# Optimization experiments

Measured on AMD Instinct MI355X. Metric: run time of the kernel, lower is better.

## Reference

```python
import jax, jax.numpy as jnp
import numpy as np

B, S, D = 2, 2048, 1024
N_HEAD, D_ATTN = 16, 64


def setup_inputs() -> dict:
    key = jax.random.key(0)
    ks = jax.random.split(key, 5)
    x = jax.random.normal(ks[0], (B, S, D), dtype=jnp.float32)
    # causal mask: True = masked (as consumed by torch.masked_fill)
    mask = jnp.triu(jnp.ones((S, S), dtype=bool), k=1)
    scale = 0.02
    w_q = jax.random.normal(ks[1], (D, N_HEAD * D_ATTN), dtype=jnp.float32) * scale
    w_k = jax.random.normal(ks[2], (D, N_HEAD * D_ATTN), dtype=jnp.float32) * scale
    w_v = jax.random.normal(ks[3], (D, N_HEAD * D_ATTN), dtype=jnp.float32) * scale
    w_o = jax.random.normal(ks[4], (N_HEAD * D_ATTN, D), dtype=jnp.float32) * scale
    return {"x": x, "mask": mask, "w_q": w_q, "w_k": w_k, "w_v": w_v, "w_o": w_o}


def _split(t):
    # [B,S,H*Da] -> [B,H,S,Da]
    b, s, _ = t.shape
    return t.reshape(b, s, N_HEAD, D_ATTN).transpose(0, 2, 1, 3)


def reference(x, mask, w_q, w_k, w_v, w_o):
    q = _split(x @ w_q)
    k = _split(x @ w_k)
    v = _split(x @ w_v)
    scale = D_ATTN ** 0.5
    score = jnp.einsum("bhqd,bhkd->bhqk", q, k) / scale  # [B,H,S,S]
    score = jnp.where(mask, -jnp.inf, score)
    prob = jax.nn.softmax(score, axis=-1)
    out = jnp.einsum("bhqk,bhkd->bhqd", prob, v)
    out = out.transpose(0, 2, 1, 3).reshape(x.shape[0], x.shape[1], N_HEAD * D_ATTN)
    return out @ w_o
```

## Files before the change

### kernel.cpp

```cpp
#include <hip/hip_runtime.h>
#include <stdint.h>

using u16 = unsigned short;
using u32 = unsigned int;
using u64 = unsigned long long;

typedef float f32x4 __attribute__((ext_vector_type(4)));
typedef __bf16 bf16x8 __attribute__((ext_vector_type(8)));

#define DEV static __device__ __forceinline__

DEV u16 f2bf(float f) {
  u32 u = __float_as_uint(f);
  u += 0x7FFFu + ((u >> 16) & 1u);
  return (u16)(u >> 16);
}

DEV void gld16(const void* g, void* l) {
  __builtin_amdgcn_global_load_lds((__attribute__((address_space(1))) void*)g,
                                   (__attribute__((address_space(3))) void*)l,
                                   16, 0, 0);
}

__global__ void k_cvt_x(const float* __restrict__ x, u16* __restrict__ xb) {
  int i = (blockIdx.x * 256 + threadIdx.x) * 8;
  float4 a = *(const float4*)&x[i];
  float4 b = *(const float4*)&x[i + 4];
  __align__(16) u16 o[8];
  o[0] = f2bf(a.x); o[1] = f2bf(a.y); o[2] = f2bf(a.z); o[3] = f2bf(a.w);
  o[4] = f2bf(b.x); o[5] = f2bf(b.y); o[6] = f2bf(b.z); o[7] = f2bf(b.w);
  *(uint4*)&xb[i] = *(const uint4*)o;
}

__global__ void k_cvt_w(const float* __restrict__ w0, const float* __restrict__ w1,
                        const float* __restrict__ w2, const float* __restrict__ w3,
                        u16* __restrict__ t0, u16* __restrict__ t1,
                        u16* __restrict__ t2, u16* __restrict__ t3) {
  const float* w = blockIdx.z == 0 ? w0 : blockIdx.z == 1 ? w1 : blockIdx.z == 2 ? w2 : w3;
  u16* wt       = blockIdx.z == 0 ? t0 : blockIdx.z == 1 ? t1 : blockIdx.z == 2 ? t2 : t3;
  __shared__ __align__(16) float tile[64][68];
  const int tid = threadIdx.x;
  const int k0 = blockIdx.x * 64, n0 = blockIdx.y * 64;
#pragma unroll
  for (int i = 0; i < 4; ++i) {
    int c = tid + i * 256;
    int kr = c >> 4, col = (c & 15) * 4;
    *(float4*)&tile[kr][col] = *(const float4*)&w[(size_t)(k0 + kr) * 1024 + n0 + col];
  }
  __syncthreads();
#pragma unroll
  for (int i = 0; i < 2; ++i) {
    int c = tid + i * 256;
    int nr = c >> 3, kc = (c & 7) * 8;
    __align__(16) u16 o[8];
#pragma unroll
    for (int j = 0; j < 8; ++j) o[j] = f2bf(tile[kc + j][nr]);
    *(uint4*)&wt[(size_t)(n0 + nr) * 1024 + k0 + kc] = *(const uint4*)o;
  }
}

DEV void gemm_mainloop(const u16* __restrict__ A, const u16* __restrict__ Bt,
                       int m0, int n0, u16* Asb, u16* Bsb, f32x4 (&acc)[4][4]) {
  const int tid = threadIdx.x;
  const int lane = tid & 63;
  const int wv = tid >> 6;
  const int wm = (wv >> 1) * 64, wn = (wv & 1) * 64;

#pragma unroll
  for (int i = 0; i < 4; ++i)
#pragma unroll
    for (int j = 0; j < 4; ++j) {
      f32x4 z = {0.f, 0.f, 0.f, 0.f};
      acc[i][j] = z;
    }

  const int c0 = wv * 64 + lane, c1 = c0 + 256;
  const int r0 = c0 >> 2, r1 = c1 >> 2;
  const int b0 = (c0 & 3) ^ (r0 & 3) ^ ((r0 >> 2) & 3);
  const int b1 = (c1 & 3) ^ (r1 & 3) ^ ((r1 >> 2) & 3);
  const u16* ga0 = A + (size_t)(m0 + r0) * 1024 + b0 * 8;
  const u16* ga1 = A + (size_t)(m0 + r1) * 1024 + b1 * 8;
  const u16* gb0 = Bt + (size_t)(n0 + r0) * 1024 + b0 * 8;
  const u16* gb1 = Bt + (size_t)(n0 + r1) * 1024 + b1 * 8;
  u16* la0 = Asb + (wv * 64) * 8;
  u16* la1 = Asb + (wv * 64 + 256) * 8;
  u16* lb0 = Bsb + (wv * 64) * 8;
  u16* lb1 = Bsb + (wv * 64 + 256) * 8;

  int aoff[4], boff[4];
#pragma unroll
  for (int f = 0; f < 4; ++f) {
    int ra = wm + f * 16 + (lane & 15);
    aoff[f] = ra * 32 + (((lane >> 4) ^ (ra & 3) ^ ((ra >> 2) & 3)) * 8);
    int rb = wn + f * 16 + (lane & 15);
    boff[f] = rb * 32 + (((lane >> 4) ^ (rb & 3) ^ ((rb >> 2) & 3)) * 8);
  }

  for (int kt = 0; kt < 32; ++kt) {
    const int k0 = kt * 32;
    gld16(ga0 + k0, la0);
    gld16(ga1 + k0, la1);
    gld16(gb0 + k0, lb0);
    gld16(gb1 + k0, lb1);
    __syncthreads();
    bf16x8 af[4], bfv[4];
#pragma unroll
    for (int f = 0; f < 4; ++f) af[f] = *(const bf16x8*)&Asb[aoff[f]];
#pragma unroll
    for (int f = 0; f < 4; ++f) bfv[f] = *(const bf16x8*)&Bsb[boff[f]];
#pragma unroll
    for (int i = 0; i < 4; ++i)
#pragma unroll
      for (int j = 0; j < 4; ++j)
        acc[i][j] = __builtin_amdgcn_mfma_f32_16x16x32_bf16(af[i], bfv[j], acc[i][j], 0, 0, 0);
    __syncthreads();
  }
}

__global__ __launch_bounds__(256) void k_gemm_qkv(
    const u16* __restrict__ X, const u16* __restrict__ Wq, const u16* __restrict__ Wk,
    const u16* __restrict__ Wv, u16* __restrict__ Q, u16* __restrict__ K,
    u16* __restrict__ V) {
  __shared__ __align__(16) u16 Asb[128 * 32];
  __shared__ __align__(16) u16 Bsb[128 * 32];
  const int nb = blockIdx.x, mb = blockIdx.y;
  const int proj = nb >> 3, n0 = (nb & 7) * 128;
  const u16* W = proj == 0 ? Wq : proj == 1 ? Wk : Wv;
  u16* Dst = proj == 0 ? Q : proj == 1 ? K : V;
  const float scl = proj == 0 ? 0.125f * 1.4426950408889634f : 1.0f;
  f32x4 acc[4][4];
  gemm_mainloop(X, W, mb * 128, n0, Asb, Bsb, acc);
  const int lane = threadIdx.x & 63, wv = threadIdx.x >> 6;
  const int wm = (wv >> 1) * 64, wn = (wv & 1) * 64;
#pragma unroll
  for (int i = 0; i < 4; ++i)
#pragma unroll
    for (int j = 0; j < 4; ++j)
#pragma unroll
      for (int r = 0; r < 4; ++r) {
        int m = mb * 128 + wm + i * 16 + (lane >> 4) * 4 + r;
        int n = n0 + wn + j * 16 + (lane & 15);
        int b = m >> 11, s = m & 2047, h = n >> 6, d = n & 63;
        Dst[(size_t)((b * 16 + h) * 2048 + s) * 64 + d] = f2bf(acc[i][j][r] * scl);
      }
}

__global__ __launch_bounds__(256) void k_gemm_out(
    const u16* __restrict__ A, const u16* __restrict__ Wt, float* __restrict__ Out) {
  __shared__ __align__(16) u16 Asb[128 * 32];
  __shared__ __align__(16) u16 Bsb[128 * 32];
  const int nb = blockIdx.x, mb = blockIdx.y;
  f32x4 acc[4][4];
  gemm_mainloop(A, Wt, mb * 128, nb * 128, Asb, Bsb, acc);
  const int lane = threadIdx.x & 63, wv = threadIdx.x >> 6;
  const int wm = (wv >> 1) * 64, wn = (wv & 1) * 64;
#pragma unroll
  for (int i = 0; i < 4; ++i)
#pragma unroll
    for (int j = 0; j < 4; ++j)
#pragma unroll
      for (int r = 0; r < 4; ++r) {
        int m = mb * 128 + wm + i * 16 + (lane >> 4) * 4 + r;
        int n = nb * 128 + wn + j * 16 + (lane & 15);
        Out[(size_t)m * 1024 + n] = acc[i][j][r];
      }
}

__global__ void k_transpose_v(const u16* __restrict__ V, u16* __restrict__ Vt) {
  __shared__ __align__(16) u16 t[64][80];
  const int bh = blockIdx.y, s0 = blockIdx.x * 64;
  const int tid = threadIdx.x;
#pragma unroll
  for (int i = 0; i < 2; ++i) {
    int c = tid + i * 256;
    int sr = c >> 3, dc = (c & 7) * 8;
    *(uint4*)&t[sr][dc] = *(const uint4*)&V[((size_t)bh * 2048 + s0 + sr) * 64 + dc];
  }
  __syncthreads();
#pragma unroll
  for (int i = 0; i < 2; ++i) {
    int c = tid + i * 256;
    int dr = c >> 3, c7 = c & 7;
    __align__(8) u16 o[8];
#pragma unroll
    for (int j = 0; j < 8; ++j) o[j] = t[c7 * 8 + j][dr];
    int bp = ((c7 >> 1) & 1) * 32 + (c7 & 1) * 16 + ((c7 >> 2) & 1) * 4;
    u16* row = &Vt[((size_t)bh * 64 + dr) * 2048 + s0];
    *(u64*)&row[bp]     = *(const u64*)&o[0];
    *(u64*)&row[bp + 8] = *(const u64*)&o[4];
  }
}

DEV void qk_tile(const u16* Kc, const bf16x8 (&qf)[2], int lo, int hi, f32x4 (&sc)[4]) {
#pragma unroll
  for (int cf = 0; cf < 4; ++cf) {
    f32x4 z = {0.f, 0.f, 0.f, 0.f};
    sc[cf] = z;
#pragma unroll
    for (int kf = 0; kf < 2; ++kf) {
      int row = cf * 16 + lo;
      int blk = ((kf * 4 + hi) ^ (row & 7)) * 8;
      bf16x8 kfr = *(const bf16x8*)&Kc[row * 64 + blk];
      sc[cf] = __builtin_amdgcn_mfma_f32_16x16x32_bf16(kfr, qf[kf], sc[cf], 0, 0, 0);
    }
  }
}

DEV void sm_pv(f32x4 (&sc)[4], const u16* Vc, int lane, int lo, int hi,
               float& m_run, float& l_run, f32x4 (&ao)[4]) {
  float mx0 = fmaxf(fmaxf(sc[0][0], sc[0][1]), fmaxf(sc[0][2], sc[0][3]));
  float mx1 = fmaxf(fmaxf(sc[1][0], sc[1][1]), fmaxf(sc[1][2], sc[1][3]));
  float mx2 = fmaxf(fmaxf(sc[2][0], sc[2][1]), fmaxf(sc[2][2], sc[2][3]));
  float mx3 = fmaxf(fmaxf(sc[3][0], sc[3][1]), fmaxf(sc[3][2], sc[3][3]));
  float mx = fmaxf(fmaxf(mx0, mx1), fmaxf(mx2, mx3));
  mx = fmaxf(mx, __shfl_xor(mx, 16));
  mx = fmaxf(mx, __shfl_xor(mx, 32));

  if (__any(mx > m_run + 8.0f)) {
    float mnew = fmaxf(m_run, mx);
    float sclf = __builtin_amdgcn_exp2f(m_run - mnew);
    const int base = lane & 48;
#pragma unroll
    for (int r = 0; r < 4; ++r) {
      float s_r = __shfl(sclf, base + hi * 4 + r);
#pragma unroll
      for (int df = 0; df < 4; ++df) ao[df][r] *= s_r;
    }
    l_run *= sclf;
    m_run = mnew;
  }

  float pp[4];
  bf16x8 pa0, pa1;
#pragma unroll
  for (int cf = 0; cf < 4; ++cf) {
    float p0 = __builtin_amdgcn_exp2f(sc[cf][0] - m_run);
    float p1 = __builtin_amdgcn_exp2f(sc[cf][1] - m_run);
    float p2 = __builtin_amdgcn_exp2f(sc[cf][2] - m_run);
    float p3 = __builtin_amdgcn_exp2f(sc[cf][3] - m_run);
    pp[cf] = (p0 + p1) + (p2 + p3);
    bf16x8& pa = (cf & 1) ? pa1 : pa0;
    int j = (cf >> 1) * 4;
    pa[j] = (__bf16)p0; pa[j + 1] = (__bf16)p1;
    pa[j + 2] = (__bf16)p2; pa[j + 3] = (__bf16)p3;
  }
  float psum = (pp[0] + pp[1]) + (pp[2] + pp[3]);
  psum += __shfl_xor(psum, 16);
  psum += __shfl_xor(psum, 32);
  l_run += psum;

  __builtin_amdgcn_s_setprio(1);
#pragma unroll
  for (int df = 0; df < 4; ++df) {
#pragma unroll
    for (int kf = 0; kf < 2; ++kf) {
      int row = df * 16 + lo;
      int blk = ((kf * 4 + hi) ^ (row & 7)) * 8;
      bf16x8 vfr = *(const bf16x8*)&Vc[row * 64 + blk];
      ao[df] = __builtin_amdgcn_mfma_f32_16x16x32_bf16(kf == 0 ? pa0 : pa1, vfr,
                                                       ao[df], 0, 0, 0);
    }
  }
  __builtin_amdgcn_s_setprio(0);
}

__global__ __launch_bounds__(512) void k_attn(
    const u16* __restrict__ Qg, const u16* __restrict__ Kg,
    const u16* __restrict__ Vtg, u16* __restrict__ Og) {
  __shared__ __align__(16) u16 Ks[2][64 * 64];
  __shared__ __align__(16) u16 Vs[2][64 * 64];
  const int tid = threadIdx.x, lane = tid & 63, wv = tid >> 6;
  const int lo = lane & 15, hi = lane >> 4;
  const int w4 = wv & 3, qsel = wv >> 2;

  const int flat = blockIdx.y * 16 + blockIdx.x;
  const int xcd = flat & 7, slot = flat >> 3;
  const int bh = xcd * 4 + (slot >> 4);
  const int jp = slot & 15;

  const u16* Qb = Qg + (size_t)bh * 2048 * 64;
  const u16* Kb = Kg + (size_t)bh * 2048 * 64;
  const u16* Vb = Vtg + (size_t)bh * 64 * 2048;
  const int b = bh >> 4, h = bh & 15;

  const int nta = jp + 1, ntb = 32 - jp;
  const int q0 = (qsel ? (31 - jp) : jp) * 64;
  const int myNt = qsel ? ntb : nta;
  const int qq = q0 + w4 * 16 + lo;

  bf16x8 qf[2];
#pragma unroll
  for (int kf = 0; kf < 2; ++kf)
    qf[kf] = *(const bf16x8*)&Qb[(size_t)(q0 + w4 * 16 + lo) * 64 + kf * 32 + hi * 8];

  f32x4 ao[4];
#pragma unroll
  for (int df = 0; df < 4; ++df) {
    f32x4 z = {0.f, 0.f, 0.f, 0.f};
    ao[df] = z;
  }
  float m_run = -1e30f, l_run = 0.f;

  const int r0 = tid >> 3;
  const int e0 = ((tid & 7) ^ (r0 & 7)) * 8;

  gld16(Kb + (size_t)r0 * 64 + e0, &Ks[0][wv * 512]);
  gld16(Vb + (size_t)r0 * 2048 + e0, &Vs[0][wv * 512]);
  __syncthreads();

#pragma unroll 1
  for (int t = 0; t < ntb; ++t) {
    const u16* Kc = Ks[t & 1];
    const u16* Vc = Vs[t & 1];
    if (t + 1 < ntb) {
      const int kn = (t + 1) * 64;
      gld16(Kb + (size_t)(kn + r0) * 64 + e0, &Ks[(t + 1) & 1][wv * 512]);
      gld16(Vb + (size_t)r0 * 2048 + kn + e0, &Vs[(t + 1) & 1][wv * 512]);
    }

    if (t < myNt) {
      f32x4 sc[4];
      __builtin_amdgcn_s_setprio(1);
      qk_tile(Kc, qf, lo, hi, sc);
      __builtin_amdgcn_s_setprio(0);

      if (t == myNt - 1) {
        const int kv0 = t * 64;
#pragma unroll
        for (int cf = 0; cf < 4; ++cf)
#pragma unroll
          for (int r = 0; r < 4; ++r) {
            int kk = kv0 + cf * 16 + hi * 4 + r;
            if (kk > qq) sc[cf][r] = -1e30f;
          }
      }

      sm_pv(sc, Vc, lane, lo, hi, m_run, l_run, ao);
    }

    __syncthreads();
  }

  float linv[4];
  const int base = lane & 48;
#pragma unroll
  for (int r = 0; r < 4; ++r) {
    float l_r = __shfl(l_run, base + hi * 4 + r);
    linv[r] = 1.0f / l_r;
  }
#pragma unroll
  for (int df = 0; df < 4; ++df)
#pragma unroll
    for (int r = 0; r < 4; ++r) {
      int s = q0 + w4 * 16 + hi * 4 + r;
      int d = df * 16 + lo;
      Og[((size_t)(b * 2048 + s)) * 1024 + h * 64 + d] = f2bf(ao[df][r] * linv[r]);
    }
}

extern "C" void kernel_launch(void* const* d_in, const int* in_sizes, int n_in,
                              void* d_out, int out_size, void* d_ws, size_t ws_size,
                              hipStream_t stream) {
  const float* x = (const float*)d_in[0];
  const float* wq = (const float*)d_in[2];
  const float* wk = (const float*)d_in[3];
  const float* wv = (const float*)d_in[4];
  const float* wo = (const float*)d_in[5];

  char* ws = (char*)d_ws;
  u16* xb  = (u16*)(ws);
  u16* wqt = (u16*)(ws + 8388608);
  u16* wkt = (u16*)(ws + 8388608 + 2097152);
  u16* wvt = (u16*)(ws + 8388608 + 2 * 2097152);
  u16* wot = (u16*)(ws + 8388608 + 3 * 2097152);
  u16* qb  = (u16*)(ws + 16777216);
  u16* kb  = (u16*)(ws + 16777216 + 8388608);
  u16* vb  = (u16*)(ws + 16777216 + 2 * 8388608);
  u16* vt  = (u16*)(ws + 16777216 + 3 * 8388608);
  u16* ao  = (u16*)(ws + 16777216 + 4 * 8388608);

  k_cvt_x<<<dim3(2048), dim3(256), 0, stream>>>(x, xb);
  k_cvt_w<<<dim3(16, 16, 4), dim3(256), 0, stream>>>(wq, wk, wv, wo, wqt, wkt, wvt, wot);
  k_gemm_qkv<<<dim3(24, 32), dim3(256), 0, stream>>>(xb, wqt, wkt, wvt, qb, kb, vb);
  k_transpose_v<<<dim3(32, 32), dim3(256), 0, stream>>>(vb, vt);
  k_attn<<<dim3(16, 32), dim3(512), 0, stream>>>(qb, kb, vt, ao);
  k_gemm_out<<<dim3(8, 32), dim3(256), 0, stream>>>(ao, wot, (float*)d_out);
}
```

Measured before the change: 122.9 us.

## Give each attention wave two query row-fragments and merge conversion kernels

The attention kernel drops from 512 to 256 threads per block. Each wave now processes 32 query rows as two 16-row fragments, so every K and V fragment read from LDS feeds two MFMAs and LDS traffic per FLOP is halved. Each thread issues twice as many async tile loads, and registers per thread roughly double for accumulators, scores and Q fragments, which may limit occupancy. Separately, the x and weight bf16 conversion kernels are merged into one launch to save a kernel launch.

```diff
diff --git a/kernel.cpp b/kernel.cpp
--- a/kernel.cpp
+++ b/kernel.cpp
@@ -22,36 +22,39 @@
                                    16, 0, 0);
 }
 
-__global__ void k_cvt_x(const float* __restrict__ x, u16* __restrict__ xb) {
-  int i = (blockIdx.x * 256 + threadIdx.x) * 8;
-  float4 a = *(const float4*)&x[i];
-  float4 b = *(const float4*)&x[i + 4];
-  __align__(16) u16 o[8];
-  o[0] = f2bf(a.x); o[1] = f2bf(a.y); o[2] = f2bf(a.z); o[3] = f2bf(a.w);
-  o[4] = f2bf(b.x); o[5] = f2bf(b.y); o[6] = f2bf(b.z); o[7] = f2bf(b.w);
-  *(uint4*)&xb[i] = *(const uint4*)o;
-}
-
-__global__ void k_cvt_w(const float* __restrict__ w0, const float* __restrict__ w1,
-                        const float* __restrict__ w2, const float* __restrict__ w3,
-                        u16* __restrict__ t0, u16* __restrict__ t1,
-                        u16* __restrict__ t2, u16* __restrict__ t3) {
-  const float* w = blockIdx.z == 0 ? w0 : blockIdx.z == 1 ? w1 : blockIdx.z == 2 ? w2 : w3;
-  u16* wt       = blockIdx.z == 0 ? t0 : blockIdx.z == 1 ? t1 : blockIdx.z == 2 ? t2 : t3;
+__global__ void k_cvt(const float* __restrict__ x, u16* __restrict__ xb,
+                      const float* __restrict__ w0, const float* __restrict__ w1,
+                      const float* __restrict__ w2, const float* __restrict__ w3,
+                      u16* __restrict__ t0, u16* __restrict__ t1,
+                      u16* __restrict__ t2, u16* __restrict__ t3) {
+  const int tid = threadIdx.x;
+  if (blockIdx.x < 2048) {
+    int i = (blockIdx.x * 256 + tid) * 8;
+    float4 a = *(const float4*)&x[i];
+    float4 b = *(const float4*)&x[i + 4];
+    __align__(16) u16 o[8];
+    o[0] = f2bf(a.x); o[1] = f2bf(a.y); o[2] = f2bf(a.z); o[3] = f2bf(a.w);
+    o[4] = f2bf(b.x); o[5] = f2bf(b.y); o[6] = f2bf(b.z); o[7] = f2bf(b.w);
+    *(uint4*)&xb[i] = *(const uint4*)o;
+    return;
+  }
+  const int c = blockIdx.x - 2048;
+  const int z = c >> 8, rem = c & 255;
+  const float* w = z == 0 ? w0 : z == 1 ? w1 : z == 2 ? w2 : w3;
+  u16* wt       = z == 0 ? t0 : z == 1 ? t1 : z == 2 ? t2 : t3;
   __shared__ __align__(16) float tile[64][68];
-  const int tid = threadIdx.x;
-  const int k0 = blockIdx.x * 64, n0 = blockIdx.y * 64;
+  const int k0 = (rem & 15) * 64, n0 = (rem >> 4) * 64;
 #pragma unroll
   for (int i = 0; i < 4; ++i) {
-    int c = tid + i * 256;
-    int kr = c >> 4, col = (c & 15) * 4;
+    int cc = tid + i * 256;
+    int kr = cc >> 4, col = (cc & 15) * 4;
     *(float4*)&tile[kr][col] = *(const float4*)&w[(size_t)(k0 + kr) * 1024 + n0 + col];
   }
   __syncthreads();
 #pragma unroll
   for (int i = 0; i < 2; ++i) {
-    int c = tid + i * 256;
-    int nr = c >> 3, kc = (c & 7) * 8;
+    int cc = tid + i * 256;
+    int nr = cc >> 3, kc = (cc & 7) * 8;
     __align__(16) u16 o[8];
 #pragma unroll
     for (int j = 0; j < 8; ++j) o[j] = f2bf(tile[kc + j][nr]);
@@ -191,87 +194,14 @@
   }
 }
 
-DEV void qk_tile(const u16* Kc, const bf16x8 (&qf)[2], int lo, int hi, f32x4 (&sc)[4]) {
-#pragma unroll
-  for (int cf = 0; cf < 4; ++cf) {
-    f32x4 z = {0.f, 0.f, 0.f, 0.f};
-    sc[cf] = z;
-#pragma unroll
-    for (int kf = 0; kf < 2; ++kf) {
-      int row = cf * 16 + lo;
-      int blk = ((kf * 4 + hi) ^ (row & 7)) * 8;
-      bf16x8 kfr = *(const bf16x8*)&Kc[row * 64 + blk];
-      sc[cf] = __builtin_amdgcn_mfma_f32_16x16x32_bf16(kfr, qf[kf], sc[cf], 0, 0, 0);
-    }
-  }
-}
-
-DEV void sm_pv(f32x4 (&sc)[4], const u16* Vc, int lane, int lo, int hi,
-               float& m_run, float& l_run, f32x4 (&ao)[4]) {
-  float mx0 = fmaxf(fmaxf(sc[0][0], sc[0][1]), fmaxf(sc[0][2], sc[0][3]));
-  float mx1 = fmaxf(fmaxf(sc[1][0], sc[1][1]), fmaxf(sc[1][2], sc[1][3]));
-  float mx2 = fmaxf(fmaxf(sc[2][0], sc[2][1]), fmaxf(sc[2][2], sc[2][3]));
-  float mx3 = fmaxf(fmaxf(sc[3][0], sc[3][1]), fmaxf(sc[3][2], sc[3][3]));
-  float mx = fmaxf(fmaxf(mx0, mx1), fmaxf(mx2, mx3));
-  mx = fmaxf(mx, __shfl_xor(mx, 16));
-  mx = fmaxf(mx, __shfl_xor(mx, 32));
-
-  if (__any(mx > m_run + 8.0f)) {
-    float mnew = fmaxf(m_run, mx);
-    float sclf = __builtin_amdgcn_exp2f(m_run - mnew);
-    const int base = lane & 48;
-#pragma unroll
-    for (int r = 0; r < 4; ++r) {
-      float s_r = __shfl(sclf, base + hi * 4 + r);
-#pragma unroll
-      for (int df = 0; df < 4; ++df) ao[df][r] *= s_r;
-    }
-    l_run *= sclf;
-    m_run = mnew;
-  }
-
-  float pp[4];
-  bf16x8 pa0, pa1;
-#pragma unroll
-  for (int cf = 0; cf < 4; ++cf) {
-    float p0 = __builtin_amdgcn_exp2f(sc[cf][0] - m_run);
-    float p1 = __builtin_amdgcn_exp2f(sc[cf][1] - m_run);
-    float p2 = __builtin_amdgcn_exp2f(sc[cf][2] - m_run);
-    float p3 = __builtin_amdgcn_exp2f(sc[cf][3] - m_run);
-    pp[cf] = (p0 + p1) + (p2 + p3);
-    bf16x8& pa = (cf & 1) ? pa1 : pa0;
-    int j = (cf >> 1) * 4;
-    pa[j] = (__bf16)p0; pa[j + 1] = (__bf16)p1;
-    pa[j + 2] = (__bf16)p2; pa[j + 3] = (__bf16)p3;
-  }
-  float psum = (pp[0] + pp[1]) + (pp[2] + pp[3]);
-  psum += __shfl_xor(psum, 16);
-  psum += __shfl_xor(psum, 32);
-  l_run += psum;
-
-  __builtin_amdgcn_s_setprio(1);
-#pragma unroll
-  for (int df = 0; df < 4; ++df) {
-#pragma unroll
-    for (int kf = 0; kf < 2; ++kf) {
-      int row = df * 16 + lo;
-      int blk = ((kf * 4 + hi) ^ (row & 7)) * 8;
-      bf16x8 vfr = *(const bf16x8*)&Vc[row * 64 + blk];
-      ao[df] = __builtin_amdgcn_mfma_f32_16x16x32_bf16(kf == 0 ? pa0 : pa1, vfr,
-                                                       ao[df], 0, 0, 0);
-    }
-  }
-  __builtin_amdgcn_s_setprio(0);
-}
-
-__global__ __launch_bounds__(512) void k_attn(
+__global__ __launch_bounds__(256, 4) void k_attn(
     const u16* __restrict__ Qg, const u16* __restrict__ Kg,
     const u16* __restrict__ Vtg, u16* __restrict__ Og) {
   __shared__ __align__(16) u16 Ks[2][64 * 64];
   __shared__ __align__(16) u16 Vs[2][64 * 64];
   const int tid = threadIdx.x, lane = tid & 63, wv = tid >> 6;
   const int lo = lane & 15, hi = lane >> 4;
-  const int w4 = wv & 3, qsel = wv >> 2;
+  const int qsel = wv >> 1, wrow = (wv & 1) * 32;
 
   const int flat = blockIdx.y * 16 + blockIdx.x;
   const int xcd = flat & 7, slot = flat >> 3;
@@ -286,26 +216,34 @@
   const int nta = jp + 1, ntb = 32 - jp;
   const int q0 = (qsel ? (31 - jp) : jp) * 64;
   const int myNt = qsel ? ntb : nta;
-  const int qq = q0 + w4 * 16 + lo;
-
-  bf16x8 qf[2];
-#pragma unroll
-  for (int kf = 0; kf < 2; ++kf)
-    qf[kf] = *(const bf16x8*)&Qb[(size_t)(q0 + w4 * 16 + lo) * 64 + kf * 32 + hi * 8];
-
-  f32x4 ao[4];
-#pragma unroll
-  for (int df = 0; df < 4; ++df) {
-    f32x4 z = {0.f, 0.f, 0.f, 0.f};
-    ao[df] = z;
-  }
-  float m_run = -1e30f, l_run = 0.f;
-
-  const int r0 = tid >> 3;
-  const int e0 = ((tid & 7) ^ (r0 & 7)) * 8;
+
+  bf16x8 qf[2][2];
+#pragma unroll
+  for (int rf = 0; rf < 2; ++rf)
+#pragma unroll
+    for (int kf = 0; kf < 2; ++kf)
+      qf[rf][kf] = *(const bf16x8*)&Qb[(size_t)(q0 + wrow + rf * 16 + lo) * 64 +
+                                       kf * 32 + hi * 8];
+
+  f32x4 ao[2][4];
+#pragma unroll
+  for (int rf = 0; rf < 2; ++rf)
+#pragma unroll
+    for (int df = 0; df < 4; ++df) {
+      f32x4 z = {0.f, 0.f, 0.f, 0.f};
+      ao[rf][df] = z;
+    }
+  float m_run[2] = {-1e30f, -1e30f}, l_run[2] = {0.f, 0.f};
+
+  const int c0 = tid, c1 = tid + 256;
+  const int r0 = c0 >> 3, r1 = c1 >> 3;
+  const int e0 = ((c0 & 7) ^ (r0 & 7)) * 8;
+  const int e1 = ((c1 & 7) ^ (r1 & 7)) * 8;
 
   gld16(Kb + (size_t)r0 * 64 + e0, &Ks[0][wv * 512]);
+  gld16(Kb + (size_t)r1 * 64 + e1, &Ks[0][wv * 512 + 2048]);
   gld16(Vb + (size_t)r0 * 2048 + e0, &Vs[0][wv * 512]);
+  gld16(Vb + (size_t)r1 * 2048 + e1, &Vs[0][wv * 512 + 2048]);
   __syncthreads();
 
 #pragma unroll 1
@@ -314,48 +252,138 @@
     const u16* Vc = Vs[t & 1];
     if (t + 1 < ntb) {
       const int kn = (t + 1) * 64;
-      gld16(Kb + (size_t)(kn + r0) * 64 + e0, &Ks[(t + 1) & 1][wv * 512]);
-      gld16(Vb + (size_t)r0 * 2048 + kn + e0, &Vs[(t + 1) & 1][wv * 512]);
+      u16* kd = Ks[(t + 1) & 1];
+      u16* vd = Vs[(t + 1) & 1];
+      gld16(Kb + (size_t)(kn + r0) * 64 + e0, kd + wv * 512);
+      gld16(Kb + (size_t)(kn + r1) * 64 + e1, kd + wv * 512 + 2048);
+      gld16(Vb + (size_t)r0 * 2048 + kn + e0, vd + wv * 512);
+      gld16(Vb + (size_t)r1 * 2048 + kn + e1, vd + wv * 512 + 2048);
     }
 
     if (t < myNt) {
-      f32x4 sc[4];
+      f32x4 sc[2][4];
       __builtin_amdgcn_s_setprio(1);
-      qk_tile(Kc, qf, lo, hi, sc);
+#pragma unroll
+      for (int cf = 0; cf < 4; ++cf) {
+        f32x4 z = {0.f, 0.f, 0.f, 0.f};
+        sc[0][cf] = z;
+        sc[1][cf] = z;
+#pragma unroll
+        for (int kf = 0; kf < 2; ++kf) {
+          int row = cf * 16 + lo;
+          int blk = ((kf * 4 + hi) ^ (row & 7)) * 8;
+          bf16x8 kfr = *(const bf16x8*)&Kc[row * 64 + blk];
+          sc[0][cf] = __builtin_amdgcn_mfma_f32_16x16x32_bf16(kfr, qf[0][kf], sc[0][cf], 0, 0, 0);
+          sc[1][cf] = __builtin_amdgcn_mfma_f32_16x16x32_bf16(kfr, qf[1][kf], sc[1][cf], 0, 0, 0);
+        }
+      }
       __builtin_amdgcn_s_setprio(0);
 
       if (t == myNt - 1) {
         const int kv0 = t * 64;
 #pragma unroll
-        for (int cf = 0; cf < 4; ++cf)
+        for (int rf = 0; rf < 2; ++rf) {
+          const int qq = q0 + wrow + rf * 16 + lo;
+#pragma unroll
+          for (int cf = 0; cf < 4; ++cf)
+#pragma unroll
+            for (int r = 0; r < 4; ++r) {
+              int kk = kv0 + cf * 16 + hi * 4 + r;
+              if (kk > qq) sc[rf][cf][r] = -1e30f;
+            }
+        }
+      }
+
+      float mx[2];
+#pragma unroll
+      for (int rf = 0; rf < 2; ++rf) {
+        float a0 = fmaxf(fmaxf(sc[rf][0][0], sc[rf][0][1]), fmaxf(sc[rf][0][2], sc[rf][0][3]));
+        float a1 = fmaxf(fmaxf(sc[rf][1][0], sc[rf][1][1]), fmaxf(sc[rf][1][2], sc[rf][1][3]));
+        float a2 = fmaxf(fmaxf(sc[rf][2][0], sc[rf][2][1]), fmaxf(sc[rf][2][2], sc[rf][2][3]));
+        float a3 = fmaxf(fmaxf(sc[rf][3][0], sc[rf][3][1]), fmaxf(sc[rf][3][2], sc[rf][3][3]));
+        float m = fmaxf(fmaxf(a0, a1), fmaxf(a2, a3));
+        m = fmaxf(m, __shfl_xor(m, 16));
+        m = fmaxf(m, __shfl_xor(m, 32));
+        mx[rf] = m;
+      }
+      if (__any(fmaxf(mx[0] - m_run[0], mx[1] - m_run[1]) > 8.0f)) {
+        const int base = lane & 48;
+#pragma unroll
+        for (int rf = 0; rf < 2; ++rf) {
+          float mnew = fmaxf(m_run[rf], mx[rf]);
+          float sclf = __builtin_amdgcn_exp2f(m_run[rf] - mnew);
 #pragma unroll
           for (int r = 0; r < 4; ++r) {
-            int kk = kv0 + cf * 16 + hi * 4 + r;
-            if (kk > qq) sc[cf][r] = -1e30f;
+            float s_r = __shfl(sclf, base + hi * 4 + r);
+#pragma unroll
+            for (int df = 0; df < 4; ++df) ao[rf][df][r] *= s_r;
           }
-      }
-
-      sm_pv(sc, Vc, lane, lo, hi, m_run, l_run, ao);
+          l_run[rf] *= sclf;
+          m_run[rf] = mnew;
+        }
+      }
+
+      bf16x8 pa[2][2];
+      float psum[2];
+#pragma unroll
+      for (int rf = 0; rf < 2; ++rf) {
+        float pp[4];
+#pragma unroll
+        for (int cf = 0; cf < 4; ++cf) {
+          float p0 = __builtin_amdgcn_exp2f(sc[rf][cf][0] - m_run[rf]);
+          float p1 = __builtin_amdgcn_exp2f(sc[rf][cf][1] - m_run[rf]);
+          float p2 = __builtin_amdgcn_exp2f(sc[rf][cf][2] - m_run[rf]);
+          float p3 = __builtin_amdgcn_exp2f(sc[rf][cf][3] - m_run[rf]);
+          pp[cf] = (p0 + p1) + (p2 + p3);
+          int j = (cf >> 1) * 4;
+          bf16x8& pax = pa[rf][cf & 1];
+          pax[j] = (__bf16)p0; pax[j + 1] = (__bf16)p1;
+          pax[j + 2] = (__bf16)p2; pax[j + 3] = (__bf16)p3;
+        }
+        float ps = (pp[0] + pp[1]) + (pp[2] + pp[3]);
+        ps += __shfl_xor(ps, 16);
+        ps += __shfl_xor(ps, 32);
+        l_run[rf] += ps;
+        psum[rf] = ps;
+      }
+      (void)psum;
+
+      __builtin_amdgcn_s_setprio(1);
+#pragma unroll
+      for (int df = 0; df < 4; ++df) {
+#pragma unroll
+        for (int kf = 0; kf < 2; ++kf) {
+          int row = df * 16 + lo;
+          int blk = ((kf * 4 + hi) ^ (row & 7)) * 8;
+          bf16x8 vfr = *(const bf16x8*)&Vc[row * 64 + blk];
+          ao[0][df] = __builtin_amdgcn_mfma_f32_16x16x32_bf16(pa[0][kf], vfr, ao[0][df], 0, 0, 0);
+          ao[1][df] = __builtin_amdgcn_mfma_f32_16x16x32_bf16(pa[1][kf], vfr, ao[1][df], 0, 0, 0);
+        }
+      }
+      __builtin_amdgcn_s_setprio(0);
     }
 
     __syncthreads();
   }
 
-  float linv[4];
   const int base = lane & 48;
 #pragma unroll
-  for (int r = 0; r < 4; ++r) {
-    float l_r = __shfl(l_run, base + hi * 4 + r);
-    linv[r] = 1.0f / l_r;
-  }
-#pragma unroll
-  for (int df = 0; df < 4; ++df)
+  for (int rf = 0; rf < 2; ++rf) {
+    float linv[4];
 #pragma unroll
     for (int r = 0; r < 4; ++r) {
-      int s = q0 + w4 * 16 + hi * 4 + r;
-      int d = df * 16 + lo;
-      Og[((size_t)(b * 2048 + s)) * 1024 + h * 64 + d] = f2bf(ao[df][r] * linv[r]);
+      float l_r = __shfl(l_run[rf], base + hi * 4 + r);
+      linv[r] = 1.0f / l_r;
     }
+#pragma unroll
+    for (int df = 0; df < 4; ++df)
+#pragma unroll
+      for (int r = 0; r < 4; ++r) {
+        int s = q0 + wrow + rf * 16 + hi * 4 + r;
+        int d = df * 16 + lo;
+        Og[((size_t)(b * 2048 + s)) * 1024 + h * 64 + d] = f2bf(ao[rf][df][r] * linv[r]);
+      }
+  }
 }
 
 extern "C" void kernel_launch(void* const* d_in, const int* in_sizes, int n_in,
@@ -379,10 +407,9 @@
   u16* vt  = (u16*)(ws + 16777216 + 3 * 8388608);
   u16* ao  = (u16*)(ws + 16777216 + 4 * 8388608);
 
-  k_cvt_x<<<dim3(2048), dim3(256), 0, stream>>>(x, xb);
-  k_cvt_w<<<dim3(16, 16, 4), dim3(256), 0, stream>>>(wq, wk, wv, wo, wqt, wkt, wvt, wot);
+  k_cvt<<<dim3(3072), dim3(256), 0, stream>>>(x, xb, wq, wk, wv, wo, wqt, wkt, wvt, wot);
   k_gemm_qkv<<<dim3(24, 32), dim3(256), 0, stream>>>(xb, wqt, wkt, wvt, qb, kb, vb);
   k_transpose_v<<<dim3(32, 32), dim3(256), 0, stream>>>(vb, vt);
-  k_attn<<<dim3(16, 32), dim3(512), 0, stream>>>(qb, kb, vt, ao);
+  k_attn<<<dim3(16, 32), dim3(256), 0, stream>>>(qb, kb, vt, ao);
   k_gemm_out<<<dim3(8, 32), dim3(256), 0, stream>>>(ao, wot, (float*)d_out);
 }
```

New measurement: 132.6 us. 7.9% more time.

## Deepen GEMM and attention load pipelines with multi-buffered LDS and merge conversion kernels

Applied to the files above, without the earlier changes.

The GEMM mainloop moves from a load-then-sync scheme to a triple-buffered LDS pipeline that keeps two tiles of async global-to-LDS loads in flight, using explicit vmcnt waits and one barrier per iteration. The attention kernel goes from double to quad buffering of K/V, prefetching three tiles ahead with counted waits and dropping the trailing syncthreads. The x and weight conversion kernels are merged into a single launch. The intent is to hide global memory latency and cut barrier and launch overhead, at the cost of more LDS per block, which may lower occupancy, and a reliance on correct hand-written vmcnt counts.

```diff
diff --git a/kernel.cpp b/kernel.cpp
--- a/kernel.cpp
+++ b/kernel.cpp
@@ -22,36 +22,39 @@
                                    16, 0, 0);
 }
 
-__global__ void k_cvt_x(const float* __restrict__ x, u16* __restrict__ xb) {
-  int i = (blockIdx.x * 256 + threadIdx.x) * 8;
-  float4 a = *(const float4*)&x[i];
-  float4 b = *(const float4*)&x[i + 4];
-  __align__(16) u16 o[8];
-  o[0] = f2bf(a.x); o[1] = f2bf(a.y); o[2] = f2bf(a.z); o[3] = f2bf(a.w);
-  o[4] = f2bf(b.x); o[5] = f2bf(b.y); o[6] = f2bf(b.z); o[7] = f2bf(b.w);
-  *(uint4*)&xb[i] = *(const uint4*)o;
-}
-
-__global__ void k_cvt_w(const float* __restrict__ w0, const float* __restrict__ w1,
-                        const float* __restrict__ w2, const float* __restrict__ w3,
-                        u16* __restrict__ t0, u16* __restrict__ t1,
-                        u16* __restrict__ t2, u16* __restrict__ t3) {
-  const float* w = blockIdx.z == 0 ? w0 : blockIdx.z == 1 ? w1 : blockIdx.z == 2 ? w2 : w3;
-  u16* wt       = blockIdx.z == 0 ? t0 : blockIdx.z == 1 ? t1 : blockIdx.z == 2 ? t2 : t3;
+__global__ void k_cvt(const float* __restrict__ x, u16* __restrict__ xb,
+                      const float* __restrict__ w0, const float* __restrict__ w1,
+                      const float* __restrict__ w2, const float* __restrict__ w3,
+                      u16* __restrict__ t0, u16* __restrict__ t1,
+                      u16* __restrict__ t2, u16* __restrict__ t3) {
+  const int tid = threadIdx.x;
+  if (blockIdx.x < 2048) {
+    int i = (blockIdx.x * 256 + tid) * 8;
+    float4 a = *(const float4*)&x[i];
+    float4 b = *(const float4*)&x[i + 4];
+    __align__(16) u16 o[8];
+    o[0] = f2bf(a.x); o[1] = f2bf(a.y); o[2] = f2bf(a.z); o[3] = f2bf(a.w);
+    o[4] = f2bf(b.x); o[5] = f2bf(b.y); o[6] = f2bf(b.z); o[7] = f2bf(b.w);
+    *(uint4*)&xb[i] = *(const uint4*)o;
+    return;
+  }
+  const int c = blockIdx.x - 2048;
+  const int z = c >> 8, rem = c & 255;
+  const float* w = z == 0 ? w0 : z == 1 ? w1 : z == 2 ? w2 : w3;
+  u16* wt       = z == 0 ? t0 : z == 1 ? t1 : z == 2 ? t2 : t3;
   __shared__ __align__(16) float tile[64][68];
-  const int tid = threadIdx.x;
-  const int k0 = blockIdx.x * 64, n0 = blockIdx.y * 64;
+  const int k0 = (rem & 15) * 64, n0 = (rem >> 4) * 64;
 #pragma unroll
   for (int i = 0; i < 4; ++i) {
-    int c = tid + i * 256;
-    int kr = c >> 4, col = (c & 15) * 4;
+    int cc = tid + i * 256;
+    int kr = cc >> 4, col = (cc & 15) * 4;
     *(float4*)&tile[kr][col] = *(const float4*)&w[(size_t)(k0 + kr) * 1024 + n0 + col];
   }
   __syncthreads();
 #pragma unroll
   for (int i = 0; i < 2; ++i) {
-    int c = tid + i * 256;
-    int nr = c >> 3, kc = (c & 7) * 8;
+    int cc = tid + i * 256;
+    int nr = cc >> 3, kc = (cc & 7) * 8;
     __align__(16) u16 o[8];
 #pragma unroll
     for (int j = 0; j < 8; ++j) o[j] = f2bf(tile[kc + j][nr]);
@@ -82,10 +85,7 @@
   const u16* ga1 = A + (size_t)(m0 + r1) * 1024 + b1 * 8;
   const u16* gb0 = Bt + (size_t)(n0 + r0) * 1024 + b0 * 8;
   const u16* gb1 = Bt + (size_t)(n0 + r1) * 1024 + b1 * 8;
-  u16* la0 = Asb + (wv * 64) * 8;
-  u16* la1 = Asb + (wv * 64 + 256) * 8;
-  u16* lb0 = Bsb + (wv * 64) * 8;
-  u16* lb1 = Bsb + (wv * 64 + 256) * 8;
+  const int da0 = (wv * 64) * 8, da1 = (wv * 64 + 256) * 8;
 
   int aoff[4], boff[4];
 #pragma unroll
@@ -96,24 +96,41 @@
     boff[f] = rb * 32 + (((lane >> 4) ^ (rb & 3) ^ ((rb >> 2) & 3)) * 8);
   }
 
+#pragma unroll
+  for (int p = 0; p < 2; ++p) {
+    const int k0 = p * 32, bo = p * 4096;
+    gld16(ga0 + k0, Asb + bo + da0);
+    gld16(ga1 + k0, Asb + bo + da1);
+    gld16(gb0 + k0, Bsb + bo + da0);
+    gld16(gb1 + k0, Bsb + bo + da1);
+  }
+
+#pragma unroll 1
   for (int kt = 0; kt < 32; ++kt) {
-    const int k0 = kt * 32;
-    gld16(ga0 + k0, la0);
-    gld16(ga1 + k0, la1);
-    gld16(gb0 + k0, lb0);
-    gld16(gb1 + k0, lb1);
-    __syncthreads();
+    if (kt < 31) asm volatile("s_waitcnt vmcnt(4)" ::: "memory");
+    else         asm volatile("s_waitcnt vmcnt(0)" ::: "memory");
+    __builtin_amdgcn_s_barrier();
+    __builtin_amdgcn_sched_barrier(0);
+
+    if (kt + 2 < 32) {
+      const int k0 = (kt + 2) * 32, bo = ((kt + 2) % 3) * 4096;
+      gld16(ga0 + k0, Asb + bo + da0);
+      gld16(ga1 + k0, Asb + bo + da1);
+      gld16(gb0 + k0, Bsb + bo + da0);
+      gld16(gb1 + k0, Bsb + bo + da1);
+    }
+
+    const int bo = (kt % 3) * 4096;
     bf16x8 af[4], bfv[4];
 #pragma unroll
-    for (int f = 0; f < 4; ++f) af[f] = *(const bf16x8*)&Asb[aoff[f]];
-#pragma unroll
-    for (int f = 0; f < 4; ++f) bfv[f] = *(const bf16x8*)&Bsb[boff[f]];
+    for (int f = 0; f < 4; ++f) af[f] = *(const bf16x8*)&Asb[bo + aoff[f]];
+#pragma unroll
+    for (int f = 0; f < 4; ++f) bfv[f] = *(const bf16x8*)&Bsb[bo + boff[f]];
 #pragma unroll
     for (int i = 0; i < 4; ++i)
 #pragma unroll
       for (int j = 0; j < 4; ++j)
         acc[i][j] = __builtin_amdgcn_mfma_f32_16x16x32_bf16(af[i], bfv[j], acc[i][j], 0, 0, 0);
-    __syncthreads();
   }
 }
 
@@ -121,8 +138,8 @@
     const u16* __restrict__ X, const u16* __restrict__ Wq, const u16* __restrict__ Wk,
     const u16* __restrict__ Wv, u16* __restrict__ Q, u16* __restrict__ K,
     u16* __restrict__ V) {
-  __shared__ __align__(16) u16 Asb[128 * 32];
-  __shared__ __align__(16) u16 Bsb[128 * 32];
+  __shared__ __align__(16) u16 Asb[3 * 4096];
+  __shared__ __align__(16) u16 Bsb[3 * 4096];
   const int nb = blockIdx.x, mb = blockIdx.y;
   const int proj = nb >> 3, n0 = (nb & 7) * 128;
   const u16* W = proj == 0 ? Wq : proj == 1 ? Wk : Wv;
@@ -147,8 +164,8 @@
 
 __global__ __launch_bounds__(256) void k_gemm_out(
     const u16* __restrict__ A, const u16* __restrict__ Wt, float* __restrict__ Out) {
-  __shared__ __align__(16) u16 Asb[128 * 32];
-  __shared__ __align__(16) u16 Bsb[128 * 32];
+  __shared__ __align__(16) u16 Asb[3 * 4096];
+  __shared__ __align__(16) u16 Bsb[3 * 4096];
   const int nb = blockIdx.x, mb = blockIdx.y;
   f32x4 acc[4][4];
   gemm_mainloop(A, Wt, mb * 128, nb * 128, Asb, Bsb, acc);
@@ -267,8 +284,8 @@
 __global__ __launch_bounds__(512) void k_attn(
     const u16* __restrict__ Qg, const u16* __restrict__ Kg,
     const u16* __restrict__ Vtg, u16* __restrict__ Og) {
-  __shared__ __align__(16) u16 Ks[2][64 * 64];
-  __shared__ __align__(16) u16 Vs[2][64 * 64];
+  __shared__ __align__(16) u16 Ks[4][64 * 64];
+  __shared__ __align__(16) u16 Vs[4][64 * 64];
   const int tid = threadIdx.x, lane = tid & 63, wv = tid >> 6;
   const int lo = lane & 15, hi = lane >> 4;
   const int w4 = wv & 3, qsel = wv >> 2;
@@ -304,21 +321,29 @@
   const int r0 = tid >> 3;
   const int e0 = ((tid & 7) ^ (r0 & 7)) * 8;
 
-  gld16(Kb + (size_t)r0 * 64 + e0, &Ks[0][wv * 512]);
-  gld16(Vb + (size_t)r0 * 2048 + e0, &Vs[0][wv * 512]);
-  __syncthreads();
+#pragma unroll
+  for (int p = 0; p < 3; ++p) {
+    gld16(Kb + (size_t)(p * 64 + r0) * 64 + e0, &Ks[p][wv * 512]);
+    gld16(Vb + (size_t)r0 * 2048 + p * 64 + e0, &Vs[p][wv * 512]);
+  }
 
 #pragma unroll 1
   for (int t = 0; t < ntb; ++t) {
-    const u16* Kc = Ks[t & 1];
-    const u16* Vc = Vs[t & 1];
-    if (t + 1 < ntb) {
-      const int kn = (t + 1) * 64;
-      gld16(Kb + (size_t)(kn + r0) * 64 + e0, &Ks[(t + 1) & 1][wv * 512]);
-      gld16(Vb + (size_t)r0 * 2048 + kn + e0, &Vs[(t + 1) & 1][wv * 512]);
+    if (t + 2 < ntb)      asm volatile("s_waitcnt vmcnt(4)" ::: "memory");
+    else if (t + 1 < ntb) asm volatile("s_waitcnt vmcnt(2)" ::: "memory");
+    else                  asm volatile("s_waitcnt vmcnt(0)" ::: "memory");
+    __builtin_amdgcn_s_barrier();
+    __builtin_amdgcn_sched_barrier(0);
+
+    if (t + 3 < ntb) {
+      const int kn = (t + 3) * 64;
+      gld16(Kb + (size_t)(kn + r0) * 64 + e0, &Ks[(t + 3) & 3][wv * 512]);
+      gld16(Vb + (size_t)r0 * 2048 + kn + e0, &Vs[(t + 3) & 3][wv * 512]);
     }
 
     if (t < myNt) {
+      const u16* Kc = Ks[t & 3];
+      const u16* Vc = Vs[t & 3];
       f32x4 sc[4];
       __builtin_amdgcn_s_setprio(1);
       qk_tile(Kc, qf, lo, hi, sc);
@@ -337,8 +362,6 @@
 
       sm_pv(sc, Vc, lane, lo, hi, m_run, l_run, ao);
     }
-
-    __syncthreads();
   }
 
   float linv[4];
@@ -379,8 +402,7 @@
   u16* vt  = (u16*)(ws + 16777216 + 3 * 8388608);
   u16* ao  = (u16*)(ws + 16777216 + 4 * 8388608);
 
-  k_cvt_x<<<dim3(2048), dim3(256), 0, stream>>>(x, xb);
-  k_cvt_w<<<dim3(16, 16, 4), dim3(256), 0, stream>>>(wq, wk, wv, wo, wqt, wkt, wvt, wot);
+  k_cvt<<<dim3(3072), dim3(256), 0, stream>>>(x, xb, wq, wk, wv, wo, wqt, wkt, wvt, wot);
   k_gemm_qkv<<<dim3(24, 32), dim3(256), 0, stream>>>(xb, wqt, wkt, wvt, qb, kb, vb);
   k_transpose_v<<<dim3(32, 32), dim3(256), 0, stream>>>(vb, vt);
   k_attn<<<dim3(16, 32), dim3(512), 0, stream>>>(qb, kb, vt, ao);
```

Measured after the change: 118.9 us. 3.2% less time.
